# Kernel tuning notes

Measured on AMD Instinct MI355X. Metric: run time of the kernel, lower is better.

## Reference

```python
import jax, jax.numpy as jnp
import numpy as np

B, S, D = 4, 8192, 768
H, HD = 12, 64
CS, NL = 512, 32


def setup_inputs() -> dict:
    key = jax.random.key(0)
    ks = jax.random.split(key, 9)
    sc = 0.02
    return {
        "x": jax.random.normal(ks[0], (B, S, D), jnp.float32),
        "q_w": jax.random.normal(ks[1], (D, D), jnp.float32) * sc,
        "q_b": jax.random.normal(ks[2], (D,), jnp.float32) * sc,
        "k_w": jax.random.normal(ks[3], (D, D), jnp.float32) * sc,
        "k_b": jax.random.normal(ks[4], (D,), jnp.float32) * sc,
        "v_w": jax.random.normal(ks[5], (D, D), jnp.float32) * sc,
        "v_b": jax.random.normal(ks[6], (D,), jnp.float32) * sc,
        "o_w": jax.random.normal(ks[7], (D, D), jnp.float32) * sc,
        "o_b": jax.random.normal(ks[8], (D,), jnp.float32) * sc,
    }


def reference(x, q_w, q_b, k_w, k_b, v_w, v_b, o_w, o_b):
    # x: (B, S, D); S divisible by CS and NL -> no padding / trimming needed.
    scale = HD ** -0.5
    n_chunks = S // CS
    seg = S // NL
    # Global landmarks: mean-pool NL evenly spaced segments. (B, NL, D)
    landmarks = x.reshape(B, NL, seg, D).mean(axis=2)
    # Q only over local tokens (torch Linear: x @ W^T + b)
    q = (x @ q_w.T + q_b).reshape(B, n_chunks, CS, H, HD)
    x_chunks = x.reshape(B, n_chunks, CS, D)
    # Prepend landmarks to every chunk's KV context: ctx = NL + CS
    lm = jnp.broadcast_to(landmarks[:, None], (B, n_chunks, NL, D))
    kv_ctx = jnp.concatenate([lm, x_chunks], axis=2)  # (B, n_chunks, ctx, D)
    ctx = NL + CS
    k = (kv_ctx @ k_w.T + k_b).reshape(B, n_chunks, ctx, H, HD)
    v = (kv_ctx @ v_w.T + v_b).reshape(B, n_chunks, ctx, H, HD)
    scores = jnp.einsum("bnqhd,bnkhd->bnhqk", q, k) * scale
    attn = jax.nn.softmax(scores, axis=-1)  # dropout=0 (eval)
    out = jnp.einsum("bnhqk,bnkhd->bnqhd", attn, v).reshape(B, S, D)
    return out @ o_w.T + o_b
```

## Files before the change

### kernel.cpp

```cpp
#include <hip/hip_runtime.h>


typedef unsigned short u16;
typedef __attribute__((ext_vector_type(8))) short short8;
typedef __attribute__((ext_vector_type(4))) float f32x4;

__device__ __forceinline__ u16 f2bf(float f) {
    unsigned u = __float_as_uint(f);
    u += 0x7fffu + ((u >> 16) & 1u);
    return (u16)(u >> 16);
}

#define MFMA_BF16(A, B, C) __builtin_amdgcn_mfma_f32_16x16x32_bf16((A), (B), (C), 0, 0, 0)

__device__ __forceinline__ void gload16(const u16* g, const short* l) {
    __builtin_amdgcn_global_load_lds(
        (__attribute__((address_space(1))) void*)g,
        (__attribute__((address_space(3))) void*)l, 16, 0, 0);
}

__global__ __launch_bounds__(256) void k_cvtx(const float* __restrict__ x,
                                              u16* __restrict__ xa,
                                              float* __restrict__ part) {
    const int g = blockIdx.x;
    const int t = threadIdx.x;
    const float* base = x + (size_t)g * 64 * 768;
    u16* ob = xa + (size_t)g * 64 * 768;
    float s0 = 0.f, s1 = 0.f, s2 = 0.f;
    for (int r = 0; r < 64; ++r) {
        const size_t off = (size_t)r * 768;
        const float v0 = base[off + t], v1 = base[off + t + 256], v2 = base[off + t + 512];
        s0 += v0; s1 += v1; s2 += v2;
        ob[off + t] = f2bf(v0); ob[off + t + 256] = f2bf(v1); ob[off + t + 512] = f2bf(v2);
    }
    float* p = part + (size_t)g * 768;
    p[t] = s0; p[t + 256] = s1; p[t + 512] = s2;
}

__global__ void k_lmred(const float* __restrict__ part, u16* __restrict__ xa_lm) {
    const int bl = blockIdx.x;
    const int t = threadIdx.x;
    const float* p = part + (size_t)bl * 4 * 768;
    const float inv = 1.f / 256.f;
    for (int c = t; c < 768; c += 256) {
        const float s = p[c] + p[768 + c] + p[1536 + c] + p[2304 + c];
        xa_lm[(size_t)bl * 768 + c] = f2bf(s * inv);
    }
}

__global__ void k_cvtw(const float* __restrict__ qw, const float* __restrict__ kw,
                       const float* __restrict__ vw, const float* __restrict__ ow,
                       const float* __restrict__ qb, const float* __restrict__ kb,
                       const float* __restrict__ vb,
                       u16* __restrict__ wcat, u16* __restrict__ owb,
                       float* __restrict__ bcat) {
    const int yy = blockIdx.y;
    const int i = blockIdx.x * 256 + threadIdx.x;
    if (yy == 4) {
        if (i < 768)       bcat[i] = qb[i];
        else if (i < 1536) bcat[i] = kb[i - 768];
        else if (i < 2304) bcat[i] = vb[i - 1536];
        return;
    }
    const float* src = (yy == 0) ? qw : (yy == 1) ? kw : (yy == 2) ? vw : ow;
    u16* dst = (yy == 3) ? owb : wcat + (size_t)yy * 589824;
    const float4 v = ((const float4*)src)[i];
    ushort4 o;
    o.x = f2bf(v.x); o.y = f2bf(v.y); o.z = f2bf(v.z); o.w = f2bf(v.w);
    ((ushort4*)dst)[i] = o;
}

template <int MODE>
__global__ __launch_bounds__(256, 2) void k_gemm(
    const u16* __restrict__ A, const u16* __restrict__ Bw, const float* __restrict__ bias,
    u16* __restrict__ qx, u16* __restrict__ ktok, u16* __restrict__ vt,
    u16* __restrict__ klm, u16* __restrict__ vlmt, float* __restrict__ outf)
{
    __shared__ short lA[2][8192];
    __shared__ short lB[2][8192];
    const int t = threadIdx.x;
    const int wid = t >> 6, lane = t & 63, lr = lane & 15, lg = lane >> 4;
    const int wm = wid >> 1, wn = wid & 1;

    const int gx = gridDim.x;
    const int nwg = gx * gridDim.y;
    const int orig = blockIdx.x + gx * blockIdx.y;
    const int qq = nwg >> 3, rr = nwg & 7, xcd = orig & 7, ii = orig >> 3;
    const int wg = (xcd < rr ? xcd * (qq + 1) : rr * (qq + 1) + (xcd - rr) * qq) + ii;
    const int m0 = (wg / gx) * 128, n0 = (wg % gx) * 128;

    const u16* pa[4]; const u16* pb[4];
#pragma unroll
    for (int j = 0; j < 4; ++j) {
        const int u = j * 256 + t;
        const int row = u >> 3, col = ((u & 7) ^ (row & 7)) * 8;
        pa[j] = A  + (size_t)(m0 + row) * 768 + col;
        pb[j] = Bw + (size_t)(n0 + row) * 768 + col;
    }
    const int sa0 = (lg ^ (lr & 7)) * 8;
    const int sa1 = ((4 + lg) ^ (lr & 7)) * 8;

#define STG(S, T) {                                                       \
    gload16(pa[0] + (T) * 64, &lA[S][0 * 2048 + wid * 512]);              \
    gload16(pb[0] + (T) * 64, &lB[S][0 * 2048 + wid * 512]);              \
    gload16(pa[1] + (T) * 64, &lA[S][1 * 2048 + wid * 512]);              \
    gload16(pb[1] + (T) * 64, &lB[S][1 * 2048 + wid * 512]);              \
    gload16(pa[2] + (T) * 64, &lA[S][2 * 2048 + wid * 512]);              \
    gload16(pb[2] + (T) * 64, &lB[S][2 * 2048 + wid * 512]);              \
    gload16(pa[3] + (T) * 64, &lA[S][3 * 2048 + wid * 512]);              \
    gload16(pb[3] + (T) * 64, &lB[S][3 * 2048 + wid * 512]); }

    f32x4 acc[4][4] = {};
    STG(0, 0);

#pragma unroll
    for (int T = 0; T < 12; ++T) {
        const int s = T & 1;
        asm volatile("s_waitcnt vmcnt(0)" ::: "memory");
        __builtin_amdgcn_s_barrier();
        __builtin_amdgcn_sched_barrier(0);
        if (T + 1 < 12) STG(s ^ 1, T + 1);
        short8 aq[4][2], bq[4][2];
#pragma unroll
        for (int mf = 0; mf < 4; ++mf) {
            const int rb = (wm * 64 + mf * 16 + lr) * 64;
            aq[mf][0] = *(const short8*)&lA[s][rb + sa0];
            aq[mf][1] = *(const short8*)&lA[s][rb + sa1];
        }
#pragma unroll
        for (int nf = 0; nf < 4; ++nf) {
            const int rb = (wn * 64 + nf * 16 + lr) * 64;
            bq[nf][0] = *(const short8*)&lB[s][rb + sa0];
            bq[nf][1] = *(const short8*)&lB[s][rb + sa1];
        }
        __builtin_amdgcn_s_setprio(1);
#pragma unroll
        for (int mf = 0; mf < 4; ++mf)
#pragma unroll
            for (int nf = 0; nf < 4; ++nf)
#pragma unroll
                for (int kf = 0; kf < 2; ++kf)
                    acc[mf][nf] = MFMA_BF16(aq[mf][kf], bq[nf][kf], acc[mf][nf]);
        __builtin_amdgcn_s_setprio(0);
    }
#undef STG

    if (MODE == 0) {
        const int region = n0 / 768;
        if (region == 2) {
#pragma unroll
            for (int nf = 0; nf < 4; ++nf) {
                const int gn = n0 + wn * 64 + nf * 16 + lr;
                const float bv = bias[gn];
                const int nn = gn - 1536;
                const int h = nn >> 6, d = nn & 63;
#pragma unroll
                for (int mf = 0; mf < 4; ++mf) {
                    const int gmb = m0 + wm * 64 + mf * 16 + lg * 4;
                    ushort4 w;
                    w.x = f2bf(acc[mf][nf][0] + bv);
                    w.y = f2bf(acc[mf][nf][1] + bv);
                    w.z = f2bf(acc[mf][nf][2] + bv);
                    w.w = f2bf(acc[mf][nf][3] + bv);
                    if (gmb < 32768) {
                        const int b = gmb >> 13, ss = gmb & 8191;
                        *(ushort4*)(vt + ((size_t)(b * 12 + h) * 64 + d) * 8192 + ss) = w;
                    } else {
                        const int ii2 = gmb - 32768;
                        const int bb = ii2 >> 5, lmr = ii2 & 31;
                        *(ushort4*)(vlmt + ((size_t)(bb * 12 + h) * 64 + d) * 32 + lmr) = w;
                    }
                }
            }
        } else {
            u16* dst = (region == 0) ? qx : ktok;
#pragma unroll
            for (int nf = 0; nf < 4; ++nf) {
                const int gn = n0 + wn * 64 + nf * 16 + lr;
                const int nn = gn - region * 768;
                const int h = nn >> 6, d = nn & 63;
                const float bv = bias[gn];
#pragma unroll
                for (int mf = 0; mf < 4; ++mf) {
                    const int gmb = m0 + wm * 64 + mf * 16 + lg * 4;
#pragma unroll
                    for (int r = 0; r < 4; ++r) {
                        const int gm = gmb + r;
                        const u16 val = f2bf(acc[mf][nf][r] + bv);
                        if (gm < 32768) {
                            const int b = gm >> 13, ss = gm & 8191;
                            dst[((size_t)(b * 12 + h) * 8192 + ss) * 64 + d] = val;
                        } else if (region == 1) {
                            const int ii2 = gm - 32768;
                            klm[((size_t)((ii2 >> 5) * 12 + h) * 32 + (ii2 & 31)) * 64 + d] = val;
                        }
                    }
                }
            }
        }
    } else {
#pragma unroll
        for (int nf = 0; nf < 4; ++nf) {
            const int gn = n0 + wn * 64 + nf * 16 + lr;
            const float bvv = bias[gn];
#pragma unroll
            for (int mf = 0; mf < 4; ++mf) {
                const int gmb = m0 + wm * 64 + mf * 16 + lg * 4;
#pragma unroll
                for (int r = 0; r < 4; ++r)
                    outf[(size_t)(gmb + r) * 768 + gn] = acc[mf][nf][r] + bvv;
            }
        }
    }
}

__global__ __launch_bounds__(256) void k_attn(
    const u16* __restrict__ q, const u16* __restrict__ ktok,
    const u16* __restrict__ klm, const u16* __restrict__ vt,
    const u16* __restrict__ vlmt, u16* __restrict__ ao)
{
    __shared__ short kls[2][32 * 72];
    __shared__ short vls[2][64 * 40];
    __shared__ short pls[4][64 * 40];
    const int t = threadIdx.x, wid = t >> 6, l = t & 63, lr = l & 15, lg = l >> 4;
    const int idx = blockIdx.x;
    const int qt = idx & 1;
    const int h  = (idx >> 1) % 12;
    const int cb = (idx >> 1) / 12;
    const int c  = cb & 15, b = cb >> 4;
    const int bh = b * 12 + h;
    const int sb = c * 512 + qt * 256 + wid * 64;

    short8 qf[4][2];
#pragma unroll
    for (int mf = 0; mf < 4; ++mf)
#pragma unroll
        for (int kf = 0; kf < 2; ++kf)
            qf[mf][kf] = *(const short8*)(q + ((size_t)bh * 8192 + sb + mf * 16 + lr) * 64
                                            + kf * 32 + lg * 8);

    f32x4 O[4][4] = {};
    float lsum[4][4] = {};

    short* pw = &pls[wid][0];
    const int kn = t >> 3, kko = (t & 7) * 8;
    const int kctx = (kn < 16) ? (kn * 2) : ((kn - 16) * 2 + 1);
    const int vd = t >> 2, vco = (t & 3) * 8;

    auto kaddr = [&](int ti) -> const u16* {
        if (ti == 0) return klm + ((size_t)bh * 32 + kctx) * 64 + kko;
        return ktok + ((size_t)bh * 8192 + c * 512 + (ti - 1) * 32 + kctx) * 64 + kko;
    };
    auto vaddr = [&](int ti) -> const u16* {
        if (ti == 0) return vlmt + ((size_t)bh * 64 + vd) * 32 + vco;
        return vt + ((size_t)bh * 64 + vd) * 8192 + c * 512 + (ti - 1) * 32 + vco;
    };

    {
        const uint4 rk0 = *(const uint4*)kaddr(0);
        const uint4 rv0 = *(const uint4*)vaddr(0);
        *(uint4*)&kls[0][kn * 72 + kko] = rk0;
        *(uint4*)&vls[0][vd * 40 + vco] = rv0;
    }
    __syncthreads();

    for (int ti = 0; ti < 17; ++ti) {
        const int cur = ti & 1, nxt = cur ^ 1;
        uint4 rk, rv;
        if (ti < 16) { rk = *(const uint4*)kaddr(ti + 1); rv = *(const uint4*)vaddr(ti + 1); }

        f32x4 sc[4][2] = {};
#pragma unroll
        for (int kf = 0; kf < 2; ++kf) {
            const short8 b0 = *(const short8*)&kls[cur][(lr)      * 72 + kf * 32 + lg * 8];
            const short8 b1 = *(const short8*)&kls[cur][(16 + lr) * 72 + kf * 32 + lg * 8];
#pragma unroll
            for (int mf = 0; mf < 4; ++mf) {
                sc[mf][0] = MFMA_BF16(qf[mf][kf], b0, sc[mf][0]);
                sc[mf][1] = MFMA_BF16(qf[mf][kf], b1, sc[mf][1]);
            }
        }

#pragma unroll
        for (int mf = 0; mf < 4; ++mf) {
#pragma unroll
            for (int r = 0; r < 4; ++r) {
                const float p0 = __expf(sc[mf][0][r] * 0.125f);
                const float p1 = __expf(sc[mf][1][r] * 0.125f);
                lsum[mf][r] += p0 + p1;
                unsigned pk;
                asm("v_cvt_pk_bf16_f32 %0, %1, %2" : "=v"(pk) : "v"(p0), "v"(p1));
                const int prow = mf * 16 + lg * 4 + r;
                ((unsigned*)pw)[prow * 20 + lr] = pk;
            }
        }

        short8 vb[4];
#pragma unroll
        for (int df = 0; df < 4; ++df)
            vb[df] = *(const short8*)&vls[cur][(df * 16 + lr) * 40 + lg * 8];
#pragma unroll
        for (int mf = 0; mf < 4; ++mf) {
            const short8 pa2 = *(const short8*)&pw[(mf * 16 + lr) * 40 + lg * 8];
#pragma unroll
            for (int df = 0; df < 4; ++df)
                O[mf][df] = MFMA_BF16(pa2, vb[df], O[mf][df]);
        }

        if (ti < 16) {
            *(uint4*)&kls[nxt][kn * 72 + kko] = rk;
            *(uint4*)&vls[nxt][vd * 40 + vco] = rv;
        }
        __syncthreads();
    }

#pragma unroll
    for (int mf = 0; mf < 4; ++mf)
#pragma unroll
        for (int r = 0; r < 4; ++r) {
            float lv = lsum[mf][r];
            lv += __shfl_xor(lv, 1); lv += __shfl_xor(lv, 2);
            lv += __shfl_xor(lv, 4); lv += __shfl_xor(lv, 8);
            const float inv = 1.f / lv;
            const int srow = sb + mf * 16 + lg * 4 + r;
#pragma unroll
            for (int df = 0; df < 4; ++df)
                ao[((size_t)b * 8192 + srow) * 768 + h * 64 + df * 16 + lr] =
                    f2bf(O[mf][df][r] * inv);
        }
}

extern "C" void kernel_launch(void* const* d_in, const int* in_sizes, int n_in,
                              void* d_out, int out_size, void* d_ws, size_t ws_size,
                              hipStream_t stream)
{
    const float* x  = (const float*)d_in[0];
    const float* qw = (const float*)d_in[1];
    const float* qb = (const float*)d_in[2];
    const float* kw = (const float*)d_in[3];
    const float* kb = (const float*)d_in[4];
    const float* vw = (const float*)d_in[5];
    const float* vb = (const float*)d_in[6];
    const float* ow = (const float*)d_in[7];
    const float* ob = (const float*)d_in[8];
    float* out = (float*)d_out;

    u16* xa     = (u16*)d_ws;
    u16* wcat   = xa + (size_t)32896 * 768;
    u16* owb    = wcat + (size_t)2304 * 768;
    float* bcat = (float*)(owb + (size_t)768 * 768);
    u16* qx     = (u16*)(bcat + 2304);
    u16* ktok   = qx   + (size_t)32768 * 768;
    u16* vt     = ktok + (size_t)32768 * 768;
    u16* klm    = vt + (size_t)32768 * 768;
    u16* vlmt   = klm + 98304;
    float* part = (float*)(vlmt + 98304);
    u16* ao     = xa;

    k_cvtx<<<512, 256, 0, stream>>>(x, xa, part);
    k_lmred<<<128, 256, 0, stream>>>(part, xa + (size_t)32768 * 768);
    k_cvtw<<<dim3(576, 5), 256, 0, stream>>>(qw, kw, vw, ow, qb, kb, vb, wcat, owb, bcat);

    k_gemm<0><<<dim3(18, 257), 256, 0, stream>>>(xa, wcat, bcat,
                                                 qx, ktok, vt, klm, vlmt, nullptr);
    k_attn<<<1536, 256, 0, stream>>>(qx, ktok, klm, vt, vlmt, ao);
    k_gemm<1><<<dim3(6, 256), 256, 0, stream>>>(ao, owb, ob,
                                                nullptr, nullptr, nullptr, nullptr, nullptr, out);
}
```

Baseline: 382.5 us.

## Widen GEMM tiles to 128x256 with 8 waves and K=32 steps, prefetched two stages ahead

The QKV and output GEMMs move from 128x128 tiles with 4 waves to 128x256 tiles with 8 waves. Each K step shrinks from 64 to 32, so the kernel runs 24 iterations and can issue loads two stages ahead with a partial vmcnt wait. A second barrier after the LDS reads allows the same buffer to be refilled right away. The swizzle and epilogue column mapping change to match. The aim is more B-tile reuse and better overlap of loads with MFMA work, at the cost of more barriers per K and a larger workgroup that may lower occupancy; it is also unclear whether the unchanged epilogue still matches the new per-wave n layout.

Measured after the change: 351.6 us. 1.09x faster.

```diff
diff --git a/kernel.cpp b/kernel.cpp
--- a/kernel.cpp
+++ b/kernel.cpp
@@ -71,76 +71,65 @@
 }
 
 template <int MODE>
-__global__ __launch_bounds__(256, 2) void k_gemm(
+__global__ __launch_bounds__(512, 4) void k_gemm(
     const u16* __restrict__ A, const u16* __restrict__ Bw, const float* __restrict__ bias,
     u16* __restrict__ qx, u16* __restrict__ ktok, u16* __restrict__ vt,
     u16* __restrict__ klm, u16* __restrict__ vlmt, float* __restrict__ outf)
 {
-    __shared__ short lA[2][8192];
+    __shared__ short lA[2][4096];
     __shared__ short lB[2][8192];
     const int t = threadIdx.x;
     const int wid = t >> 6, lane = t & 63, lr = lane & 15, lg = lane >> 4;
-    const int wm = wid >> 1, wn = wid & 1;
+    const int wm = wid >> 2, wn = wid & 3;
 
     const int gx = gridDim.x;
     const int nwg = gx * gridDim.y;
     const int orig = blockIdx.x + gx * blockIdx.y;
     const int qq = nwg >> 3, rr = nwg & 7, xcd = orig & 7, ii = orig >> 3;
     const int wg = (xcd < rr ? xcd * (qq + 1) : rr * (qq + 1) + (xcd - rr) * qq) + ii;
-    const int m0 = (wg / gx) * 128, n0 = (wg % gx) * 128;
-
-    const u16* pa[4]; const u16* pb[4];
-#pragma unroll
-    for (int j = 0; j < 4; ++j) {
-        const int u = j * 256 + t;
-        const int row = u >> 3, col = ((u & 7) ^ (row & 7)) * 8;
-        pa[j] = A  + (size_t)(m0 + row) * 768 + col;
-        pb[j] = Bw + (size_t)(n0 + row) * 768 + col;
-    }
-    const int sa0 = (lg ^ (lr & 7)) * 8;
-    const int sa1 = ((4 + lg) ^ (lr & 7)) * 8;
-
-#define STG(S, T) {                                                       \
-    gload16(pa[0] + (T) * 64, &lA[S][0 * 2048 + wid * 512]);              \
-    gload16(pb[0] + (T) * 64, &lB[S][0 * 2048 + wid * 512]);              \
-    gload16(pa[1] + (T) * 64, &lA[S][1 * 2048 + wid * 512]);              \
-    gload16(pb[1] + (T) * 64, &lB[S][1 * 2048 + wid * 512]);              \
-    gload16(pa[2] + (T) * 64, &lA[S][2 * 2048 + wid * 512]);              \
-    gload16(pb[2] + (T) * 64, &lB[S][2 * 2048 + wid * 512]);              \
-    gload16(pa[3] + (T) * 64, &lA[S][3 * 2048 + wid * 512]);              \
-    gload16(pb[3] + (T) * 64, &lB[S][3 * 2048 + wid * 512]); }
+    const int m0 = (wg / gx) * 128, n0 = (wg % gx) * 256;
+
+    const int rA = t >> 2,        cA = ((t & 3) ^ ((rA >> 1) & 3)) * 8;
+    const int rB0 = t >> 2,       cB0 = cA;
+    const int uB1 = 512 + t;
+    const int rB1 = uB1 >> 2,     cB1 = (((uB1) & 3) ^ ((rB1 >> 1) & 3)) * 8;
+    const u16* pa0 = A  + (size_t)(m0 + rA) * 768 + cA;
+    const u16* pb0 = Bw + (size_t)(n0 + rB0) * 768 + cB0;
+    const u16* pb1 = Bw + (size_t)(n0 + rB1) * 768 + cB1;
+    const int sa = (lg ^ ((lr >> 1) & 3)) * 8;
+
+#define STG(S, T) {                                            \
+    gload16(pa0 + (T) * 32, &lA[S][wid * 512]);                \
+    gload16(pb0 + (T) * 32, &lB[S][wid * 512]);                \
+    gload16(pb1 + (T) * 32, &lB[S][4096 + wid * 512]); }
 
     f32x4 acc[4][4] = {};
-    STG(0, 0);
-
-#pragma unroll
-    for (int T = 0; T < 12; ++T) {
+    STG(0, 0); STG(1, 1);
+
+#pragma unroll
+    for (int T = 0; T < 24; ++T) {
         const int s = T & 1;
-        asm volatile("s_waitcnt vmcnt(0)" ::: "memory");
+        if (T < 23) asm volatile("s_waitcnt vmcnt(3)" ::: "memory");
+        else        asm volatile("s_waitcnt vmcnt(0)" ::: "memory");
         __builtin_amdgcn_s_barrier();
         __builtin_amdgcn_sched_barrier(0);
-        if (T + 1 < 12) STG(s ^ 1, T + 1);
-        short8 aq[4][2], bq[4][2];
-#pragma unroll
-        for (int mf = 0; mf < 4; ++mf) {
-            const int rb = (wm * 64 + mf * 16 + lr) * 64;
-            aq[mf][0] = *(const short8*)&lA[s][rb + sa0];
-            aq[mf][1] = *(const short8*)&lA[s][rb + sa1];
-        }
-#pragma unroll
-        for (int nf = 0; nf < 4; ++nf) {
-            const int rb = (wn * 64 + nf * 16 + lr) * 64;
-            bq[nf][0] = *(const short8*)&lB[s][rb + sa0];
-            bq[nf][1] = *(const short8*)&lB[s][rb + sa1];
-        }
+        short8 aq[4], bq[4];
+#pragma unroll
+        for (int mf = 0; mf < 4; ++mf)
+            aq[mf] = *(const short8*)&lA[s][(wm * 64 + mf * 16 + lr) * 32 + sa];
+#pragma unroll
+        for (int nf = 0; nf < 4; ++nf)
+            bq[nf] = *(const short8*)&lB[s][(wn * 64 + nf * 16 + lr) * 32 + sa];
+        asm volatile("s_waitcnt lgkmcnt(0)" ::: "memory");
+        __builtin_amdgcn_sched_barrier(0);
+        __builtin_amdgcn_s_barrier();
+        if (T + 2 < 24) STG(s, T + 2);
         __builtin_amdgcn_s_setprio(1);
 #pragma unroll
         for (int mf = 0; mf < 4; ++mf)
 #pragma unroll
             for (int nf = 0; nf < 4; ++nf)
-#pragma unroll
-                for (int kf = 0; kf < 2; ++kf)
-                    acc[mf][nf] = MFMA_BF16(aq[mf][kf], bq[nf][kf], acc[mf][nf]);
+                acc[mf][nf] = MFMA_BF16(aq[mf], bq[nf], acc[mf][nf]);
         __builtin_amdgcn_s_setprio(0);
     }
 #undef STG
@@ -361,9 +350,9 @@
     k_lmred<<<128, 256, 0, stream>>>(part, xa + (size_t)32768 * 768);
     k_cvtw<<<dim3(576, 5), 256, 0, stream>>>(qw, kw, vw, ow, qb, kb, vb, wcat, owb, bcat);
 
-    k_gemm<0><<<dim3(18, 257), 256, 0, stream>>>(xa, wcat, bcat,
-                                                 qx, ktok, vt, klm, vlmt, nullptr);
+    k_gemm<0><<<dim3(9, 257), 512, 0, stream>>>(xa, wcat, bcat,
+                                                qx, ktok, vt, klm, vlmt, nullptr);
     k_attn<<<1536, 256, 0, stream>>>(qx, ktok, klm, vt, vlmt, ao);
-    k_gemm<1><<<dim3(6, 256), 256, 0, stream>>>(ao, owb, ob,
+    k_gemm<1><<<dim3(3, 256), 512, 0, stream>>>(ao, owb, ob,
                                                 nullptr, nullptr, nullptr, nullptr, nullptr, out);
 }
```
